# Kernel tuning notes

Measured on AMD Instinct MI355X. Metric: run time of the kernel, lower is better.

The kernel has to match this reference:

```python
import jax, jax.numpy as jnp
import numpy as np

B, T, D = 16, 4096, 768   # batch, seq, feature dim (HuBERT-base)
C = 1024                  # number of k-means clusters


def setup_inputs() -> dict:
    key = jax.random.key(0)
    k_feat, k_clu = jax.random.split(key)
    feat = jax.random.normal(k_feat, (B, T, D), dtype=jnp.float32)
    clusters = jax.random.normal(k_clu, (C, D), dtype=jnp.float32)  # learned centroids [C, D]
    return {"feat": feat, "clusters": clusters}


def reference(feat, clusters):
    # feat2indice: nearest-centroid assignment.
    # torch.cdist(p=2).argmin(-1) == argmin of squared euclidean distance,
    # so we avoid the sqrt and the broadcasted [B,C,D] centroid tensor by
    x2 = jnp.sum(feat * feat, axis=-1, keepdims=True)          # [B,T,1]
    c2 = jnp.sum(clusters * clusters, axis=-1)                 # [C]
    xc = jnp.einsum('btd,cd->btc', feat, clusters)             # [B,T,C]
    d2 = x2 + c2 - 2.0 * xc                                    # [B,T,C] squared dists
    indices = jnp.argmin(d2, axis=-1)                          # [B,T] int
    return indices
```

## Files before the change

### kernel.cpp

```cpp
#include <hip/hip_runtime.h>


#define D_DIM 768
#define BM 128
#define BN 128
#define BK 32

__global__ __launch_bounds__(256) void c2_kernel(const float* __restrict__ clusters,
                                                 float* __restrict__ c2) {
    const int wave = threadIdx.x >> 6;
    const int lane = threadIdx.x & 63;
    const int c = blockIdx.x * 4 + wave;
    const float4* row = (const float4*)(clusters + (size_t)c * D_DIM);
    float s = 0.0f;
    #pragma unroll
    for (int k4 = 0; k4 < D_DIM / 4 / 64; ++k4) {
        float4 v = row[k4 * 64 + lane];
        s += v.x * v.x + v.y * v.y + v.z * v.z + v.w * v.w;
    }
    #pragma unroll
    for (int off = 32; off > 0; off >>= 1) s += __shfl_down(s, off, 64);
    if (lane == 0) c2[c] = s;
}

__global__ __launch_bounds__(256, 2) void argmin_kernel(const float* __restrict__ feat,
                                                        const float* __restrict__ clusters,
                                                        const float* __restrict__ c2,
                                                        int* __restrict__ out) {
    __shared__ float As[BK][BM];
    __shared__ float Bs[BK][BN];

    const int t  = threadIdx.x;
    const int tx = t & 15;
    const int ty = t >> 4;
    const int row0 = blockIdx.x * BM;

    const int st_r_base = t >> 3;
    const int st_kc     = (t & 7) * 4;
    const int st_xor    = (t & 7) << 2;

    float bestv[8];
    int   besti[8];
    #pragma unroll
    for (int i = 0; i < 8; ++i) { bestv[i] = 3.4e38f; besti[i] = 0; }

    for (int ct = 0; ct < 8; ++ct) {
        const int col0 = ct * BN;
        float acc[8][8];
        #pragma unroll
        for (int i = 0; i < 8; ++i)
            #pragma unroll
            for (int j = 0; j < 8; ++j) acc[i][j] = 0.0f;

        for (int k0 = 0; k0 < D_DIM; k0 += BK) {
            __syncthreads();
            #pragma unroll
            for (int i = 0; i < 4; ++i) {
                const int r  = i * 32 + st_r_base;
                const float4 v = *(const float4*)(feat + (size_t)(row0 + r) * D_DIM + k0 + st_kc);
                const int rs = r ^ st_xor;
                As[st_kc + 0][rs] = v.x;
                As[st_kc + 1][rs] = v.y;
                As[st_kc + 2][rs] = v.z;
                As[st_kc + 3][rs] = v.w;
            }
            #pragma unroll
            for (int i = 0; i < 4; ++i) {
                const int r  = i * 32 + st_r_base;
                const float4 v = *(const float4*)(clusters + (size_t)(col0 + r) * D_DIM + k0 + st_kc);
                const int rs = r ^ st_xor;
                Bs[st_kc + 0][rs] = v.x;
                Bs[st_kc + 1][rs] = v.y;
                Bs[st_kc + 2][rs] = v.z;
                Bs[st_kc + 3][rs] = v.w;
            }
            __syncthreads();

            #pragma unroll
            for (int kk = 0; kk < BK; ++kk) {
                const int xr = ((kk >> 2) & 7) << 2;
                const float4 a0 = *(const float4*)&As[kk][(ty * 8)     ^ xr];
                const float4 a1 = *(const float4*)&As[kk][(ty * 8 + 4) ^ xr];
                const float4 b0 = *(const float4*)&Bs[kk][(tx * 8)     ^ xr];
                const float4 b1 = *(const float4*)&Bs[kk][(tx * 8 + 4) ^ xr];
                float a[8] = {a0.x, a0.y, a0.z, a0.w, a1.x, a1.y, a1.z, a1.w};
                float b[8] = {b0.x, b0.y, b0.z, b0.w, b1.x, b1.y, b1.z, b1.w};
                #pragma unroll
                for (int i = 0; i < 8; ++i)
                    #pragma unroll
                    for (int j = 0; j < 8; ++j)
                        acc[i][j] = fmaf(a[i], b[j], acc[i][j]);
            }
        }

        #pragma unroll
        for (int j = 0; j < 8; ++j) {
            const int col = col0 + tx * 8 + j;
            const float cc = c2[col];
            #pragma unroll
            for (int i = 0; i < 8; ++i) {
                const float score = fmaf(-2.0f, acc[i][j], cc);
                if (score < bestv[i]) { bestv[i] = score; besti[i] = col; }
            }
        }
    }

    __syncthreads();
    float (*rv)[16] = (float(*)[16])As;
    int   (*ri)[16] = (int(*)[16])Bs;
    #pragma unroll
    for (int i = 0; i < 8; ++i) {
        rv[ty * 8 + i][tx] = bestv[i];
        ri[ty * 8 + i][tx] = besti[i];
    }
    __syncthreads();
    if (t < BM) {
        float bv = rv[t][0];
        int   bi = ri[t][0];
        #pragma unroll
        for (int x = 1; x < 16; ++x) {
            const float v  = rv[t][x];
            const int   ix = ri[t][x];
            if (v < bv || (v == bv && ix < bi)) { bv = v; bi = ix; }
        }
        out[row0 + t] = bi;
    }
}

extern "C" void kernel_launch(void* const* d_in, const int* in_sizes, int n_in,
                              void* d_out, int out_size, void* d_ws, size_t ws_size,
                              hipStream_t stream) {
    const float* feat     = (const float*)d_in[0];
    const float* clusters = (const float*)d_in[1];
    int*   out = (int*)d_out;
    float* c2  = (float*)d_ws;

    const int M = in_sizes[0] / D_DIM;
    const int C = in_sizes[1] / D_DIM;

    c2_kernel<<<C / 4, 256, 0, stream>>>(clusters, c2);
    argmin_kernel<<<M / BM, 256, 0, stream>>>(feat, clusters, c2, out);
}
```

Before: 1.397 ms.

## Use bf16 MFMA approximate argmin with top-3 margin and fp32 rescoring

Replaces the fp32 FMA GEMM with a bf16 MFMA (16x16x32) GEMM that keeps the top-3 candidate scores per row. Rows where the gap between first and second exceeds a fixed margin are accepted directly. Rows where only the third is clear get an fp32 recheck of two candidates, and ambiguous rows get a full fp32 rescan. The goal is to cut the FP32 compute cost, at the price of correctness that depends on the fixed 2.0 margin bounding the bf16 error, and on how many rows fall back to the extra passes.

```diff
diff --git a/kernel.cpp b/kernel.cpp
--- a/kernel.cpp
+++ b/kernel.cpp
@@ -1,10 +1,14 @@
 #include <hip/hip_runtime.h>
+#include <hip/hip_bf16.h>
 
 
 #define D_DIM 768
-#define BM 128
-#define BN 128
-#define BK 32
+#define MARGIN 2.0f
+#define LIGHTF (1 << 20)
+#define HEAVYF (1 << 21)
+
+typedef short bf16x8 __attribute__((ext_vector_type(8)));
+typedef float f32x4  __attribute__((ext_vector_type(4)));
 
 __global__ __launch_bounds__(256) void c2_kernel(const float* __restrict__ clusters,
                                                  float* __restrict__ c2) {
@@ -23,107 +27,245 @@
     if (lane == 0) c2[c] = s;
 }
 
-__global__ __launch_bounds__(256, 2) void argmin_kernel(const float* __restrict__ feat,
+struct Stage { float4 a0, a1; };
+
+__device__ inline Stage ldst(const float* p) {
+    Stage s;
+    s.a0 = *(const float4*)p;
+    s.a1 = *(const float4*)(p + 4);
+    return s;
+}
+
+__device__ inline void wrst(short* dst, const Stage& s) {
+    union { __hip_bfloat162 h2[4]; bf16x8 v8; } u;
+    u.h2[0] = __float22bfloat162_rn(float2{s.a0.x, s.a0.y});
+    u.h2[1] = __float22bfloat162_rn(float2{s.a0.z, s.a0.w});
+    u.h2[2] = __float22bfloat162_rn(float2{s.a1.x, s.a1.y});
+    u.h2[3] = __float22bfloat162_rn(float2{s.a1.z, s.a1.w});
+    *(bf16x8*)dst = u.v8;
+}
+
+__device__ inline void merge3(float& v1, int& i1, float& v2, int& i2, float& v3,
+                              float ov1, int oi1, float ov2, int oi2, float ov3) {
+    float m1, m2, m3; int j1, j2;
+    if (ov1 < v1) {
+        m1 = ov1; j1 = oi1;
+        if (v1 <= ov2) { m2 = v1;  j2 = i1;  m3 = fminf(ov2, v2); }
+        else           { m2 = ov2; j2 = oi2; m3 = fminf(ov3, v1); }
+    } else {
+        m1 = v1; j1 = i1;
+        if (ov1 <= v2) { m2 = ov1; j2 = oi1; m3 = fminf(v2, ov2); }
+        else           { m2 = v2;  j2 = i2;  m3 = fminf(v3, ov1); }
+    }
+    v1 = m1; i1 = j1; v2 = m2; i2 = j2; v3 = m3;
+}
+
+__global__ __launch_bounds__(256, 2) void approx_kernel(const float* __restrict__ feat,
                                                         const float* __restrict__ clusters,
-                                                        const float* __restrict__ c2,
+                                                        const float* __restrict__ c2v,
                                                         int* __restrict__ out) {
-    __shared__ float As[BK][BM];
-    __shared__ float Bs[BK][BN];
-
-    const int t  = threadIdx.x;
-    const int tx = t & 15;
-    const int ty = t >> 4;
-    const int row0 = blockIdx.x * BM;
-
-    const int st_r_base = t >> 3;
-    const int st_kc     = (t & 7) * 4;
-    const int st_xor    = (t & 7) << 2;
-
-    float bestv[8];
-    int   besti[8];
-    #pragma unroll
-    for (int i = 0; i < 8; ++i) { bestv[i] = 3.4e38f; besti[i] = 0; }
+    __shared__ short As[4096];
+    __shared__ short Bs[4096];
+    __shared__ float redv[1280];
+
+    const int t    = threadIdx.x;
+    const int lane = t & 63;
+    const int wid  = t >> 6;
+    const int wr   = wid >> 1, wc = wid & 1;
+    const int row0 = blockIdx.x * 128;
+
+    const int sl   = t & 63;
+    const int sfi  = t >> 6;
+    const int srow = sl & 15;
+    const int skof = (sl >> 4) * 8;
+
+    const float* aBase0 = feat + (size_t)(row0 + sfi * 16 + srow) * D_DIM + skof;
+    const float* aBase1 = feat + (size_t)(row0 + (sfi + 4) * 16 + srow) * D_DIM + skof;
+
+    float v1[16], v2[16], v3[16]; int i1[16], i2[16];
+    #pragma unroll
+    for (int s = 0; s < 16; ++s) { v1[s] = v2[s] = v3[s] = 3.4e38f; i1[s] = i2[s] = 0; }
+
+    const float* aptr0 = aBase0;
+    const float* aptr1 = aBase1;
 
     for (int ct = 0; ct < 8; ++ct) {
-        const int col0 = ct * BN;
-        float acc[8][8];
-        #pragma unroll
-        for (int i = 0; i < 8; ++i)
-            #pragma unroll
-            for (int j = 0; j < 8; ++j) acc[i][j] = 0.0f;
-
-        for (int k0 = 0; k0 < D_DIM; k0 += BK) {
+        const float* bptr0 = clusters + (size_t)(ct * 128 + sfi * 16 + srow) * D_DIM + skof;
+        const float* bptr1 = clusters + (size_t)(ct * 128 + (sfi + 4) * 16 + srow) * D_DIM + skof;
+
+        f32x4 acc[4][4];
+        #pragma unroll
+        for (int i = 0; i < 4; ++i)
+            #pragma unroll
+            for (int j = 0; j < 4; ++j) acc[i][j] = f32x4{0.f, 0.f, 0.f, 0.f};
+
+        Stage sA0 = ldst(aptr0), sA1 = ldst(aptr1);
+        Stage sB0 = ldst(bptr0), sB1 = ldst(bptr1);
+
+        for (int k0 = 0; k0 < D_DIM; k0 += 32) {
             __syncthreads();
-            #pragma unroll
-            for (int i = 0; i < 4; ++i) {
-                const int r  = i * 32 + st_r_base;
-                const float4 v = *(const float4*)(feat + (size_t)(row0 + r) * D_DIM + k0 + st_kc);
-                const int rs = r ^ st_xor;
-                As[st_kc + 0][rs] = v.x;
-                As[st_kc + 1][rs] = v.y;
-                As[st_kc + 2][rs] = v.z;
-                As[st_kc + 3][rs] = v.w;
-            }
-            #pragma unroll
-            for (int i = 0; i < 4; ++i) {
-                const int r  = i * 32 + st_r_base;
-                const float4 v = *(const float4*)(clusters + (size_t)(col0 + r) * D_DIM + k0 + st_kc);
-                const int rs = r ^ st_xor;
-                Bs[st_kc + 0][rs] = v.x;
-                Bs[st_kc + 1][rs] = v.y;
-                Bs[st_kc + 2][rs] = v.z;
-                Bs[st_kc + 3][rs] = v.w;
-            }
+            wrst(As + t * 8, sA0);  wrst(As + t * 8 + 2048, sA1);
+            wrst(Bs + t * 8, sB0);  wrst(Bs + t * 8 + 2048, sB1);
             __syncthreads();
-
-            #pragma unroll
-            for (int kk = 0; kk < BK; ++kk) {
-                const int xr = ((kk >> 2) & 7) << 2;
-                const float4 a0 = *(const float4*)&As[kk][(ty * 8)     ^ xr];
-                const float4 a1 = *(const float4*)&As[kk][(ty * 8 + 4) ^ xr];
-                const float4 b0 = *(const float4*)&Bs[kk][(tx * 8)     ^ xr];
-                const float4 b1 = *(const float4*)&Bs[kk][(tx * 8 + 4) ^ xr];
-                float a[8] = {a0.x, a0.y, a0.z, a0.w, a1.x, a1.y, a1.z, a1.w};
-                float b[8] = {b0.x, b0.y, b0.z, b0.w, b1.x, b1.y, b1.z, b1.w};
+            if (k0 + 32 < D_DIM) {
+                aptr0 += 32; aptr1 += 32; bptr0 += 32; bptr1 += 32;
+                sA0 = ldst(aptr0); sA1 = ldst(aptr1);
+                sB0 = ldst(bptr0); sB1 = ldst(bptr1);
+            }
+            bf16x8 a[4], b[4];
+            #pragma unroll
+            for (int i = 0; i < 4; ++i) a[i] = *(const bf16x8*)&As[((wr * 4 + i) * 64 + lane) * 8];
+            #pragma unroll
+            for (int j = 0; j < 4; ++j) b[j] = *(const bf16x8*)&Bs[((wc * 4 + j) * 64 + lane) * 8];
+            #pragma unroll
+            for (int i = 0; i < 4; ++i)
                 #pragma unroll
-                for (int i = 0; i < 8; ++i)
-                    #pragma unroll
-                    for (int j = 0; j < 8; ++j)
-                        acc[i][j] = fmaf(a[i], b[j], acc[i][j]);
-            }
-        }
-
-        #pragma unroll
-        for (int j = 0; j < 8; ++j) {
-            const int col = col0 + tx * 8 + j;
-            const float cc = c2[col];
-            #pragma unroll
-            for (int i = 0; i < 8; ++i) {
-                const float score = fmaf(-2.0f, acc[i][j], cc);
-                if (score < bestv[i]) { bestv[i] = score; besti[i] = col; }
-            }
-        }
-    }
-
+                for (int j = 0; j < 4; ++j)
+                    acc[i][j] = __builtin_amdgcn_mfma_f32_16x16x32_bf16(a[i], b[j], acc[i][j], 0, 0, 0);
+        }
+        aptr0 -= 736; aptr1 -= 736;
+
+        #pragma unroll
+        for (int j = 0; j < 4; ++j) {
+            const int col = ct * 128 + wc * 64 + j * 16 + (lane & 15);
+            const float cc = c2v[col];
+            #pragma unroll
+            for (int i = 0; i < 4; ++i)
+                #pragma unroll
+                for (int r = 0; r < 4; ++r) {
+                    const float sc = fmaf(-2.0f, acc[i][j][r], cc);
+                    const int s = i * 4 + r;
+                    if (sc < v1[s])      { v3[s]=v2[s]; v2[s]=v1[s]; i2[s]=i1[s]; v1[s]=sc; i1[s]=col; }
+                    else if (sc < v2[s]) { v3[s]=v2[s]; v2[s]=sc; i2[s]=col; }
+                    else if (sc < v3[s]) { v3[s]=sc; }
+                }
+        }
+    }
+
+    #pragma unroll
+    for (int m = 1; m < 16; m <<= 1) {
+        #pragma unroll
+        for (int s = 0; s < 16; ++s) {
+            float ov1 = __shfl_xor(v1[s], m, 64);
+            int   oi1 = __shfl_xor(i1[s], m, 64);
+            float ov2 = __shfl_xor(v2[s], m, 64);
+            int   oi2 = __shfl_xor(i2[s], m, 64);
+            float ov3 = __shfl_xor(v3[s], m, 64);
+            merge3(v1[s], i1[s], v2[s], i2[s], v3[s], ov1, oi1, ov2, oi2, ov3);
+        }
+    }
+
+    if ((lane & 15) == 0) {
+        const int g = lane >> 4;
+        #pragma unroll
+        for (int i = 0; i < 4; ++i)
+            #pragma unroll
+            for (int r = 0; r < 4; ++r) {
+                const int rowl = wr * 64 + i * 16 + g * 4 + r;
+                float* e = &redv[(rowl * 2 + wc) * 5];
+                const int s = i * 4 + r;
+                e[0] = v1[s]; e[1] = __int_as_float(i1[s]);
+                e[2] = v2[s]; e[3] = __int_as_float(i2[s]); e[4] = v3[s];
+            }
+    }
     __syncthreads();
-    float (*rv)[16] = (float(*)[16])As;
-    int   (*ri)[16] = (int(*)[16])Bs;
-    #pragma unroll
-    for (int i = 0; i < 8; ++i) {
-        rv[ty * 8 + i][tx] = bestv[i];
-        ri[ty * 8 + i][tx] = besti[i];
-    }
-    __syncthreads();
-    if (t < BM) {
-        float bv = rv[t][0];
-        int   bi = ri[t][0];
-        #pragma unroll
-        for (int x = 1; x < 16; ++x) {
-            const float v  = rv[t][x];
-            const int   ix = ri[t][x];
-            if (v < bv || (v == bv && ix < bi)) { bv = v; bi = ix; }
-        }
-        out[row0 + t] = bi;
+
+    if (t < 128) {
+        const float* e0 = &redv[(t * 2 + 0) * 5];
+        const float* e1 = &redv[(t * 2 + 1) * 5];
+        float fv1 = e0[0]; int fi1 = __float_as_int(e0[1]);
+        float fv2 = e0[2]; int fi2 = __float_as_int(e0[3]); float fv3 = e0[4];
+        merge3(fv1, fi1, fv2, fi2, fv3,
+               e1[0], __float_as_int(e1[1]), e1[2], __float_as_int(e1[3]), e1[4]);
+        int res;
+        if (fv2 - fv1 >= MARGIN)      res = fi1;
+        else if (fv3 - fv1 >= MARGIN) res = fi1 | (fi2 << 10) | LIGHTF;
+        else                          res = fi1 | HEAVYF;
+        out[row0 + t] = res;
+    }
+}
+
+__global__ __launch_bounds__(256) void light_kernel(const float* __restrict__ feat,
+                                                    const float* __restrict__ clusters,
+                                                    const float* __restrict__ c2v,
+                                                    int* __restrict__ out) {
+    const int wid  = threadIdx.x >> 6;
+    const int lane = threadIdx.x & 63;
+    const int rbase = (blockIdx.x * 4 + wid) * 16;
+    for (int rr = 0; rr < 16; ++rr) {
+        const int row = rbase + rr;
+        const int enc = out[row];
+        if (!(enc & LIGHTF)) continue;
+        const int ia = enc & 1023, ib = (enc >> 10) & 1023;
+        const float* fr = feat + (size_t)row * D_DIM + lane * 12;
+        const float4 x0 = *(const float4*)fr;
+        const float4 x1 = *(const float4*)(fr + 4);
+        const float4 x2 = *(const float4*)(fr + 8);
+        float d[2];
+        const int cs[2] = {ia, ib};
+        #pragma unroll
+        for (int q = 0; q < 2; ++q) {
+            const float* cr = clusters + (size_t)cs[q] * D_DIM + lane * 12;
+            const float4 y0 = *(const float4*)cr;
+            const float4 y1 = *(const float4*)(cr + 4);
+            const float4 y2 = *(const float4*)(cr + 8);
+            float p = x0.x * y0.x;
+            p = fmaf(x0.y, y0.y, p); p = fmaf(x0.z, y0.z, p); p = fmaf(x0.w, y0.w, p);
+            p = fmaf(x1.x, y1.x, p); p = fmaf(x1.y, y1.y, p); p = fmaf(x1.z, y1.z, p);
+            p = fmaf(x1.w, y1.w, p); p = fmaf(x2.x, y2.x, p); p = fmaf(x2.y, y2.y, p);
+            p = fmaf(x2.z, y2.z, p); p = fmaf(x2.w, y2.w, p);
+            #pragma unroll
+            for (int m = 1; m < 64; m <<= 1) p += __shfl_xor(p, m, 64);
+            d[q] = p;
+        }
+        const float sa = c2v[ia] - 2.0f * d[0];
+        const float sb = c2v[ib] - 2.0f * d[1];
+        const int res = (sb < sa || (sb == sa && ib < ia)) ? ib : ia;
+        if (lane == 0) out[row] = res;
+    }
+}
+
+__global__ __launch_bounds__(256) void heavy_kernel(const float* __restrict__ feat,
+                                                    const float* __restrict__ clusters,
+                                                    const float* __restrict__ c2v,
+                                                    int* __restrict__ out) {
+    __shared__ float frow[768];
+    __shared__ float rv[256];
+    __shared__ int   ridx[256];
+    const int t = threadIdx.x;
+    for (int rr = 0; rr < 8; ++rr) {
+        const int row = blockIdx.x * 8 + rr;
+        const int enc = out[row];
+        if (!(enc & HEAVYF)) continue;
+        for (int i = t; i < 192; i += 256)
+            *(float4*)&frow[i * 4] = *(const float4*)(feat + (size_t)row * D_DIM + i * 4);
+        __syncthreads();
+        float bv = 3.4e38f; int bi = 0;
+        for (int c = t; c < 1024; c += 256) {
+            const float* cr = clusters + (size_t)c * D_DIM;
+            float dsum = 0.0f;
+            #pragma unroll 4
+            for (int k = 0; k < 768; k += 4) {
+                const float4 y = *(const float4*)(cr + k);
+                dsum = fmaf(frow[k],     y.x, dsum);
+                dsum = fmaf(frow[k + 1], y.y, dsum);
+                dsum = fmaf(frow[k + 2], y.z, dsum);
+                dsum = fmaf(frow[k + 3], y.w, dsum);
+            }
+            const float sc = c2v[c] - 2.0f * dsum;
+            if (sc < bv) { bv = sc; bi = c; }
+        }
+        rv[t] = bv; ridx[t] = bi;
+        __syncthreads();
+        for (int s = 128; s > 0; s >>= 1) {
+            if (t < s) {
+                const float v = rv[t + s]; const int ix = ridx[t + s];
+                if (v < rv[t] || (v == rv[t] && ix < ridx[t])) { rv[t] = v; ridx[t] = ix; }
+            }
+            __syncthreads();
+        }
+        if (t == 0) out[row] = ridx[0];
+        __syncthreads();
     }
 }
 
@@ -139,5 +281,7 @@
     const int C = in_sizes[1] / D_DIM;
 
     c2_kernel<<<C / 4, 256, 0, stream>>>(clusters, c2);
-    argmin_kernel<<<M / BM, 256, 0, stream>>>(feat, clusters, c2, out);
-}
+    approx_kernel<<<M / 128, 256, 0, stream>>>(feat, clusters, c2, out);
+    light_kernel<<<M / 64, 256, 0, stream>>>(feat, clusters, c2, out);
+    heavy_kernel<<<M / 8, 256, 0, stream>>>(feat, clusters, c2, out);
+}
```

Result: slower. 2.912 ms (+108.5%).
